# Kernel optimization log

Hardware: AMD Instinct MI355X
Metric: run time of the kernel (lower is better)

The kernel has to match this reference:

```python
import jax, jax.numpy as jnp
import numpy as np

DIM = 512; H = 8; KH = 2; G = 4; DH = 64        # dim, q heads, kv heads, GQA group, head dim
BALL = 128; SEL = 64; TOPK = 2; PDIM = 3        # sliding ball, compress/selection block, topk, pos dim
SCALE = DH ** -0.5


def _rms_norm(x, gamma):
    return x * jax.lax.rsqrt(jnp.mean(x * x, axis=-1, keepdims=True) + 1e-6) * gamma


def _rotary(t):
    # t: (B, h, S, DH); GPT-NeoX style rotate-half rotary embedding
    S = t.shape[-2]
    inv = 1.0 / (10000.0 ** (jnp.arange(0, DH, 2, dtype=jnp.float32) / DH))
    f = jnp.arange(S, dtype=jnp.float32)[:, None] * inv          # (S, DH/2)
    cos = jnp.concatenate([jnp.cos(f), jnp.cos(f)], -1)
    sin = jnp.concatenate([jnp.sin(f), jnp.sin(f)], -1)
    t1, t2 = jnp.split(t, 2, -1)
    return t * cos + jnp.concatenate([-t2, t1], -1) * sin


def _forward(x, pos, pe_w, pe_b, gamma, wq, wk, wv, k_pos, v_pos,
             k_w1, k_b1, k_w2, k_b2, v_w1, v_b1, v_w2, v_b2,
             mem_k, mem_v, w_combine, w_out, num_batches):
    B = num_batches
    # relative position of leaves wrt ball center (no-grad in original)
    p = jax.lax.stop_gradient(pos).reshape(-1, SEL, PDIM)
    rel = (p - p.mean(axis=1, keepdims=True)).reshape(-1, PDIM)
    x = x + rel @ pe_w + pe_b
    x = x.reshape(B, -1, DIM)
    S = x.shape[1]
    nb = S // SEL
    h = _rms_norm(x, gamma)
    q = (h @ wq).reshape(B, S, H, DH).transpose(0, 2, 1, 3)      # (B,H,S,DH)
    k = (h @ wk).reshape(B, S, KH, DH).transpose(0, 2, 1, 3)     # (B,KH,S,DH)
    v = (h @ wv).reshape(B, S, KH, DH).transpose(0, 2, 1, 3)
    qr, kr = _rotary(q), _rotary(k)

    # --- compressed branch: per-block intra-pos emb + MLP compression ---
    kb = k.reshape(B, KH, nb, SEL, DH) + k_pos[None, :, None]
    vb = v.reshape(B, KH, nb, SEL, DH) + v_pos[None, :, None]
    ck = jax.nn.relu(kb.reshape(B, KH, nb, SEL * DH) @ k_w1 + k_b1) @ k_w2 + k_b2
    cv = jax.nn.relu(vb.reshape(B, KH, nb, SEL * DH) @ v_w1 + v_b1) @ v_w2 + v_b2
    ck = jnp.concatenate([jnp.broadcast_to(mem_k[None], (B, KH, 1, DH)), ck], axis=2)
    cv = jnp.concatenate([jnp.broadcast_to(mem_v[None], (B, KH, 1, DH)), cv], axis=2)
    qg = qr.reshape(B, KH, G, S, DH)
    csim = jnp.einsum('bkgsd,bknd->bkgsn', qg, ck) * SCALE
    cattn = jax.nn.softmax(csim, axis=-1)
    cout = jnp.einsum('bkgsn,bknd->bkgsd', cattn, cv).reshape(B, H, S, DH)

    # --- top-k block selection from compressed attention importance ---
    imp = cattn[..., 1:].mean(axis=2)                            # share over grouped q heads: (B,KH,S,nb)
    imp_blk = imp.reshape(B, KH, nb, SEL, nb).mean(axis=3)       # per query block: (B,KH,nb,nb)
    _, sel = jax.lax.top_k(imp_blk, TOPK)                        # (B,KH,nb,TOPK)

    # --- fine branch: each query block attends own + TOPK selected blocks ---
    kblk = kr.reshape(B, KH, nb, SEL, DH)
    vblk = v.reshape(B, KH, nb, SEL, DH)
    gather = jax.vmap(jax.vmap(lambda t, s: t[s]))               # (nb,SEL,DH),(nb,TOPK)->(nb,TOPK,SEL,DH)
    fk = jnp.concatenate([gather(kblk, sel), kblk[:, :, :, None]], axis=3)
    fv = jnp.concatenate([gather(vblk, sel), vblk[:, :, :, None]], axis=3)
    fk = fk.reshape(B, KH, nb, (TOPK + 1) * SEL, DH)
    fv = fv.reshape(B, KH, nb, (TOPK + 1) * SEL, DH)
    qb = qr.reshape(B, KH, G, nb, SEL, DH)
    fsim = jnp.einsum('bkgnqd,bknmd->bkgnqm', qb, fk) * SCALE
    fout = jnp.einsum('bkgnqm,bknmd->bkgnqd', jax.nn.softmax(fsim, -1), fv)
    fout = fout.reshape(B, H, S, DH)

    # --- sliding branch: MiniBallAttn = plain SDPA within balls of size 128 ---
    nw = S // BALL
    qw = qr.reshape(B, H, nw, BALL, DH)
    kw = jnp.repeat(kr, G, axis=1).reshape(B, H, nw, BALL, DH)
    vw = jnp.repeat(v, G, axis=1).reshape(B, H, nw, BALL, DH)
    ssim = jnp.einsum('bhnqd,bhnkd->bhnqk', qw, kw) * SCALE
    sout = jnp.einsum('bhnqk,bhnkd->bhnqd', jax.nn.softmax(ssim, -1), vw)
    sout = sout.reshape(B, H, S, DH)

    # --- sigmoid-gated strategy combine, merge heads, out projection ---
    gates = jax.nn.sigmoid(h @ w_combine).reshape(B, S, H, 3).transpose(0, 2, 1, 3)
    out = gates[..., 0:1] * cout + gates[..., 1:2] * fout + gates[..., 2:3] * sout
    out = out.transpose(0, 2, 1, 3).reshape(B, S, H * DH) @ w_out
    return out.reshape(-1, DIM)


def setup_inputs() -> dict:
    key = jax.random.key(0)
    ks = jax.random.split(key, 16)
    Bn, S = 8, 4096
    N = Bn * S
    CD = SEL * DH
    def lin(k, fi, fo):
        return (jax.random.normal(k, (fi, fo), jnp.float32) / np.sqrt(fi)).astype(jnp.float32)
    return {
        'x': jax.random.normal(ks[0], (N, DIM), jnp.float32),
        'pos': jax.random.normal(ks[1], (N, PDIM), jnp.float32),
        'pe_w': lin(ks[2], PDIM, DIM),
        'pe_b': jnp.zeros((DIM,), jnp.float32),
        'gamma': jnp.ones((DIM,), jnp.float32),
        'wq': lin(ks[3], DIM, H * DH),
        'wk': lin(ks[4], DIM, KH * DH),
        'wv': lin(ks[5], DIM, KH * DH),
        'k_pos': jax.random.normal(ks[6], (KH, SEL, DH), jnp.float32) * 0.02,
        'v_pos': jax.random.normal(ks[7], (KH, SEL, DH), jnp.float32) * 0.02,
        'k_w1': lin(ks[8], CD, CD), 'k_b1': jnp.zeros((CD,), jnp.float32),
        'k_w2': lin(ks[9], CD, DH), 'k_b2': jnp.zeros((DH,), jnp.float32),
        'v_w1': lin(ks[10], CD, CD), 'v_b1': jnp.zeros((CD,), jnp.float32),
        'v_w2': lin(ks[11], CD, DH), 'v_b2': jnp.zeros((DH,), jnp.float32),
        'mem_k': jax.random.normal(ks[12], (KH, 1, DH), jnp.float32) * 0.02,
        'mem_v': jax.random.normal(ks[13], (KH, 1, DH), jnp.float32) * 0.02,
        'w_combine': lin(ks[14], DIM, 3 * H),
        'w_out': lin(ks[15], H * DH, DIM),
        'num_batches': 8,
    }


def reference(x, pos, pe_w, pe_b, gamma, wq, wk, wv, k_pos, v_pos,
              k_w1, k_b1, k_w2, k_b2, v_w1, v_b1, v_w2, v_b2,
              mem_k, mem_v, w_combine, w_out, num_batches):
    return _forward(x, pos, pe_w, pe_b, gamma, wq, wk, wv, k_pos, v_pos,
                    k_w1, k_b1, k_w2, k_b2, v_w1, v_b1, v_w2, v_b2,
                    mem_k, mem_v, w_combine, w_out, num_batches)
```

## Files before the change

kernel.cpp:

```cpp
#include <hip/hip_runtime.h>
#include <stdint.h>

#define DEVI static __device__ __forceinline__
typedef unsigned short u16;
typedef __bf16 bhalf8 __attribute__((ext_vector_type(8)));
typedef float f32x4 __attribute__((ext_vector_type(4)));

DEVI u16 f2bf(float f) {
  union { float f; unsigned u; } v; v.f = f;
  unsigned r = v.u + 0x7FFFu + ((v.u >> 16) & 1u);
  return (u16)(r >> 16);
}
DEVI float bf2f(u16 h) {
  union { unsigned u; float f; } v; v.u = ((unsigned)h) << 16;
  return v.f;
}
DEVI f32x4 MFMA(bhalf8 a, bhalf8 b, f32x4 c) {
  return __builtin_amdgcn_mfma_f32_16x16x32_bf16(a, b, c, 0, 0, 0);
}
DEVI bhalf8 LD8(const u16* p) { return *(const bhalf8*)p; }
DEVI f32x4 zero4() { f32x4 z = {0.f, 0.f, 0.f, 0.f}; return z; }

#define GLDS16(gp, lp) __builtin_amdgcn_global_load_lds( \
    (const __attribute__((address_space(1))) void*)(gp), \
    (__attribute__((address_space(3))) void*)(lp), 16, 0, 0)


__global__ __launch_bounds__(256) void nsa_hnorm(const float* __restrict__ x, const float* __restrict__ pos,
    const float* __restrict__ pew, const float* __restrict__ peb,
    const float* __restrict__ gamma, u16* __restrict__ hhi, u16* __restrict__ hlo) {
  int n = blockIdx.x, t = threadIdx.x;
  int blk = n >> 6;
  __shared__ float spm[3];
  if (t < 64) {
    const float* p = pos + (size_t)(blk * 64 + t) * 3;
    float a = p[0], b = p[1], c = p[2];
#pragma unroll
    for (int o = 32; o; o >>= 1) { a += __shfl_down(a, o); b += __shfl_down(b, o); c += __shfl_down(c, o); }
    if (t == 0) { spm[0] = a * (1.f/64.f); spm[1] = b * (1.f/64.f); spm[2] = c * (1.f/64.f); }
  }
  __syncthreads();
  float r0 = pos[(size_t)n*3+0] - spm[0];
  float r1 = pos[(size_t)n*3+1] - spm[1];
  float r2 = pos[(size_t)n*3+2] - spm[2];
  int c0 = t, c1 = t + 256;
  const float* xr = x + (size_t)n * 512;
  float v0 = xr[c0] + r0*pew[c0] + r1*pew[512+c0] + r2*pew[1024+c0] + peb[c0];
  float v1 = xr[c1] + r0*pew[c1] + r1*pew[512+c1] + r2*pew[1024+c1] + peb[c1];
  float ss = v0*v0 + v1*v1;
#pragma unroll
  for (int o = 32; o; o >>= 1) ss += __shfl_down(ss, o);
  __shared__ float red[4];
  if ((t & 63) == 0) red[t >> 6] = ss;
  __syncthreads();
  float rms = 1.0f / sqrtf((red[0]+red[1]+red[2]+red[3]) * (1.0f/512.0f) + 1e-6f);
  float h0 = v0 * rms * gamma[c0], h1 = v1 * rms * gamma[c1];
  u16 a0 = f2bf(h0); hhi[(size_t)n*512+c0] = a0; hlo[(size_t)n*512+c0] = f2bf(h0 - bf2f(a0));
  u16 a1 = f2bf(h1); hhi[(size_t)n*512+c1] = a1; hlo[(size_t)n*512+c1] = f2bf(h1 - bf2f(a1));
}

__global__ __launch_bounds__(256) void nsa_wcat_rope(const float* __restrict__ wq, const float* __restrict__ wk,
    const float* __restrict__ wv, const float* __restrict__ wc, u16* __restrict__ hi, u16* __restrict__ lo,
    float* __restrict__ ct, float* __restrict__ st) {
  int bidx = blockIdx.x;
  if (bidx < 1792) {
    int idx = bidx * 256 + threadIdx.x;
    int k = idx & 511, n = idx >> 9;
    float v;
    if (n < 512) v = wq[(size_t)k*512 + n];
    else if (n < 640) v = wk[(size_t)k*128 + n - 512];
    else if (n < 768) v = wv[(size_t)k*128 + n - 640];
    else if (n < 792) v = wc[(size_t)k*24 + n - 768];
    else v = 0.f;
    u16 h = f2bf(v); hi[idx] = h; lo[idx] = f2bf(v - bf2f(h));
  } else {
    int idx = (bidx - 1792) * 256 + threadIdx.x;
    int s = idx >> 5, i = idx & 31;
    float e = (float)(2*i) * (1.0f/64.0f);
    float inv = 1.0f / powf(10000.0f, e);
    float f = (float)s * inv;
    ct[idx] = cosf(f); st[idx] = sinf(f);
  }
}

__global__ __launch_bounds__(256) void nsa_vT16(const u16* __restrict__ v16, u16* __restrict__ vT) {
  int blk = blockIdx.x;
  int st = (blk & 63) * 64, bkh = blk >> 6;
  __shared__ u16 tile[64][72];
  int t = threadIdx.x;
  int s = t >> 2, c0 = (t & 3) * 16;
  const u16* src = v16 + ((size_t)bkh*4096 + st + s) * 64;
  *(int4*)&tile[s][c0]   = *(const int4*)&src[c0];
  *(int4*)&tile[s][c0+8] = *(const int4*)&src[c0+8];
  __syncthreads();
  int d = t >> 2, s0 = (t & 3) * 16;
  u16* dst = vT + ((size_t)bkh*64 + d)*4096 + st + s0;
#pragma unroll
  for (int j = 0; j < 16; ++j) dst[j] = tile[s0+j][d];
}

__global__ __launch_bounds__(256) void nsa_wT(const float* __restrict__ src, u16* __restrict__ dhi,
    u16* __restrict__ dlo, int K, int N) {
  __shared__ float tile[64][65];
  int k0 = blockIdx.x * 64, n0 = blockIdx.y * 64;
  int t = threadIdx.x, r = t >> 2, c0 = (t & 3) * 16;
#pragma unroll
  for (int j = 0; j < 16; ++j) tile[r][c0+j] = src[(size_t)(k0+r)*N + n0 + c0 + j];
  __syncthreads();
  size_t ob = (size_t)(n0 + r)*K + k0 + c0;
#pragma unroll
  for (int j = 0; j < 16; ++j) {
    float v = tile[c0+j][r];
    u16 h = f2bf(v); dhi[ob+j] = h;
    if (dlo) dlo[ob+j] = f2bf(v - bf2f(h));
  }
}

__global__ __launch_bounds__(256) void nsa_wT2(const float* __restrict__ srcA, u16* __restrict__ dhA,
    u16* __restrict__ dlA, const float* __restrict__ srcB, u16* __restrict__ dhB, u16* __restrict__ dlB,
    int K, int N) {
  const float* src = blockIdx.z ? srcB : srcA;
  u16* dhi = blockIdx.z ? dhB : dhA;
  u16* dlo = blockIdx.z ? dlB : dlA;
  __shared__ float tile[64][65];
  int k0 = blockIdx.x * 64, n0 = blockIdx.y * 64;
  int t = threadIdx.x, r = t >> 2, c0 = (t & 3) * 16;
#pragma unroll
  for (int j = 0; j < 16; ++j) tile[r][c0+j] = src[(size_t)(k0+r)*N + n0 + c0 + j];
  __syncthreads();
  size_t ob = (size_t)(n0 + r)*K + k0 + c0;
#pragma unroll
  for (int j = 0; j < 16; ++j) {
    float v = tile[c0+j][r];
    u16 h = f2bf(v); dhi[ob+j] = h;
    if (dlo) dlo[ob+j] = f2bf(v - bf2f(h));
  }
}

__global__ __launch_bounds__(256) void nsa_red_ckcv(const float* __restrict__ part,
    const float* __restrict__ mem_k, const float* __restrict__ kb2,
    const float* __restrict__ mem_v, const float* __restrict__ vb2,
    u16* __restrict__ ckh, u16* __restrict__ ckl, u16* __restrict__ cvT) {
  int idx = blockIdx.x * 256 + threadIdx.x;
  if (idx < 81920) {
    int d = idx & 63, n = (idx >> 6) % 80, bkh = idx / (80*64);
    int kh = bkh & 1;
    float v;
    if (n == 0) v = mem_k[kh*64 + d];
    else if (n <= 64) {
      v = kb2[d];
      int m = bkh*64 + (n - 1);
#pragma unroll
      for (int kc = 0; kc < 16; ++kc) v += part[((size_t)kc*1024 + m)*64 + d];
    } else v = 0.f;
    u16 h = f2bf(v); ckh[idx] = h; ckl[idx] = f2bf(v - bf2f(h));
  } else if (idx < 81920 + 98304) {
    int j = idx - 81920;
    int cc = j % 96, d = (j / 96) & 63, bkh = j / (96*64);
    int kh = bkh & 1;
    const float* pv = part + (size_t)16*1024*64;
    float v;
    if (cc == 0) v = mem_v[kh*64 + d];
    else if (cc <= 64) {
      v = vb2[d];
      int m = bkh*64 + (cc - 1);
#pragma unroll
      for (int kc = 0; kc < 16; ++kc) v += pv[((size_t)kc*1024 + m)*64 + d];
    } else v = 0.f;
    cvT[j] = f2bf(v);
  }
}

__global__ __launch_bounds__(256) void nsa_sentinel(float* __restrict__ o, int n, float val) {
  int i = blockIdx.x * 256 + threadIdx.x;
  if (i < n) o[i] = val;
}

template<bool SPLIT, int EPI>
__global__ __launch_bounds__(256) void nsa_gemm(const u16* __restrict__ Ah, const u16* __restrict__ Al,
    const u16* __restrict__ Bh, const u16* __restrict__ Bl, int K, int N,
    const float* __restrict__ p_cos, float* __restrict__ p_sin,
    u16* __restrict__ out_hi, u16* __restrict__ out_lo, float* __restrict__ og,
    const float* __restrict__ kpos, const float* __restrict__ vpos,
    u16* __restrict__ krb, u16* __restrict__ kbh, u16* __restrict__ kbl,
    u16* __restrict__ v16o, u16* __restrict__ vbh) {
  constexpr int NB = SPLIT ? 4 : 2;
  __shared__ u16 sm[NB * 2 * 4096];
  const int t = threadIdx.x, w = t >> 6, l = t & 63;
  const int wm = w >> 1, wn = w & 1;
  int m0, n0;
  if constexpr (EPI == 0) {
    const int nper = (int)gridDim.y;
    const int bid = blockIdx.y * 256 + blockIdx.x;
    const int xcd = bid & 7, j = bid >> 3;
    const int mg = j / (8*nper), rem = j % (8*nper);
    const int nn = rem >> 3, mi = rem & 7;
    m0 = ((xcd * 4 + mg) * 8 + mi) * 128;
    n0 = nn * 128;
  } else {
    const int MBn = gridDim.x;
    const int nwg = MBn * gridDim.y;
    const int bid = blockIdx.y * MBn + blockIdx.x;
    const int swz = (bid & 7) * (nwg >> 3) + (bid >> 3);
    m0 = (swz % MBn) * 128; n0 = (swz / MBn) * 128;
  }
  const bool dsp = SPLIT && (EPI != 0 || n0 <= 512);
  const int row = l & 15;
  const int kc8 = ((l >> 4) ^ ((l >> 1) & 3)) * 8;
  const int gsc = ((l & 3) ^ ((l >> 3) & 3)) * 8;
  const int sr = l >> 2;
  f32x4 acc[4][4];
#pragma unroll
  for (int a = 0; a < 4; ++a)
#pragma unroll
    for (int b = 0; b < 4; ++b) acc[a][b] = zero4();

  auto STAGE = [&](int buf, int k0) {
    u16* base = sm + buf * NB * 4096;
#pragma unroll
    for (int s2 = 0; s2 < 2; ++s2) {
      int seg = w*2 + s2;
      int r = seg*16 + sr;
      size_t ga = (size_t)(m0 + r)*K + k0 + gsc;
      size_t gb = (size_t)(n0 + r)*K + k0 + gsc;
      GLDS16(&Ah[ga], base + seg*512);
      GLDS16(&Bh[gb], base + 4096 + seg*512);
      if (SPLIT && dsp) {
        GLDS16(&Al[ga], base + 2*4096 + seg*512);
        GLDS16(&Bl[gb], base + 3*4096 + seg*512);
      }
    }
  };

  const int nt = K >> 5;
  STAGE(0, 0);
  __syncthreads();
  int cur = 0;
  for (int kt = 0; kt < nt; ++kt) {
    if (kt + 1 < nt) STAGE(cur ^ 1, (kt + 1) * 32);
    u16* bA  = sm + cur * NB * 4096;
    u16* bB  = bA + 4096;
    u16* bAl = bA + 2*4096;
    u16* bBl = bA + 3*4096;
    bhalf8 af[4], afl[4];
#pragma unroll
    for (int mf = 0; mf < 4; ++mf) {
      af[mf] = LD8(&bA[(wm*64 + mf*16 + row)*32 + kc8]);
      if (dsp) afl[mf] = LD8(&bAl[(wm*64 + mf*16 + row)*32 + kc8]);
    }
#pragma unroll
    for (int nf = 0; nf < 4; ++nf) {
      bhalf8 bfh = LD8(&bB[(wn*64 + nf*16 + row)*32 + kc8]);
      bhalf8 bfl;
      if (dsp) bfl = LD8(&bBl[(wn*64 + nf*16 + row)*32 + kc8]);
#pragma unroll
      for (int mf = 0; mf < 4; ++mf) {
        acc[mf][nf] = MFMA(af[mf], bfh, acc[mf][nf]);
        if (dsp) {
          acc[mf][nf] = MFMA(af[mf], bfl, acc[mf][nf]);
          acc[mf][nf] = MFMA(afl[mf], bfh, acc[mf][nf]);
        }
      }
    }
    __syncthreads();
    cur ^= 1;
  }
  if constexpr (EPI == 0) {
    if (n0 < 512) {
#pragma unroll
      for (int mf = 0; mf < 4; ++mf)
#pragma unroll
        for (int i = 0; i < 4; ++i) {
          int r = m0 + wm*64 + mf*16 + (l >> 4)*4 + i;
          int s = r & 4095, b = r >> 12;
#pragma unroll
          for (int nf = 0; nf < 2; ++nf) {
            int c = n0 + wn*64 + nf*16 + (l & 15);
            int hq = c >> 6, dd = c & 31;
            float t1 = acc[mf][nf][i], t2 = acc[mf][nf+2][i];
            float cs = p_cos[s*32 + dd], sn = p_sin[s*32 + dd];
            float o1 = t1*cs - t2*sn, o2 = t2*cs + t1*sn;
            size_t ob = (((size_t)(b*8 + hq))*4096 + s)*64;
            u16 h1 = f2bf(o1); out_hi[ob+dd] = h1;    out_lo[ob+dd] = f2bf(o1 - bf2f(h1));
            u16 h2 = f2bf(o2); out_hi[ob+dd+32] = h2; out_lo[ob+dd+32] = f2bf(o2 - bf2f(h2));
          }
        }
    } else if (n0 == 512) {
      int kh = wn;
#pragma unroll
      for (int mf = 0; mf < 4; ++mf)
#pragma unroll
        for (int i = 0; i < 4; ++i) {
          int r = m0 + wm*64 + mf*16 + (l >> 4)*4 + i;
          int s = r & 4095, b = r >> 12;
          int n = s >> 6, sl = s & 63;
          size_t krbase = ((size_t)(b*2 + kh)*4096 + s)*64;
          size_t kbbase = ((size_t)(b*128 + kh*64 + n))*4096 + sl*64;
#pragma unroll
          for (int nf = 0; nf < 2; ++nf) {
            int dd = nf*16 + (l & 15);
            float t1 = acc[mf][nf][i], t2 = acc[mf][nf+2][i];
            float cs = p_cos[s*32 + dd], sn = p_sin[s*32 + dd];
            krb[krbase + dd]      = f2bf(t1*cs - t2*sn);
            krb[krbase + dd + 32] = f2bf(t2*cs + t1*sn);
          }
#pragma unroll
          for (int nf = 0; nf < 4; ++nf) {
            int dk = nf*16 + (l & 15);
            float v = acc[mf][nf][i] + kpos[(kh*64 + sl)*64 + dk];
            u16 h = f2bf(v);
            kbh[kbbase + dk] = h;
            kbl[kbbase + dk] = f2bf(v - bf2f(h));
          }
        }
    } else if (n0 == 640) {
      int kh = wn;
#pragma unroll
      for (int mf = 0; mf < 4; ++mf)
#pragma unroll
        for (int i = 0; i < 4; ++i) {
          int r = m0 + wm*64 + mf*16 + (l >> 4)*4 + i;
          int s = r & 4095, b = r >> 12;
          int n = s >> 6, sl = s & 63;
          size_t v16base = ((size_t)(b*2 + kh)*4096 + s)*64;
          size_t vbbase = ((size_t)(b*128 + kh*64 + n))*4096 + sl*64;
#pragma unroll
          for (int nf = 0; nf < 4; ++nf) {
            int dv = nf*16 + (l & 15);
            float vv = acc[mf][nf][i];
            v16o[v16base + dv] = f2bf(vv);
            vbh[vbbase + dv] = f2bf(vv + vpos[(kh*64 + sl)*64 + dv]);
          }
        }
    } else {
#pragma unroll
      for (int mf = 0; mf < 4; ++mf)
#pragma unroll
        for (int nf = 0; nf < 4; ++nf)
#pragma unroll
          for (int i = 0; i < 4; ++i) {
            int r = m0 + wm*64 + mf*16 + (l >> 4)*4 + i;
            int c = n0 + wn*64 + nf*16 + (l & 15);
            if (c < 792) og[(size_t)r*24 + (c - 768)] = 1.0f / (1.0f + expf(-acc[mf][nf][i]));
          }
    }
  } else {
#pragma unroll
    for (int mf = 0; mf < 4; ++mf)
#pragma unroll
      for (int nf = 0; nf < 4; ++nf)
#pragma unroll
        for (int i = 0; i < 4; ++i) {
          int r = m0 + wm*64 + mf*16 + (l >> 4)*4 + i;
          int c = n0 + wn*64 + nf*16 + (l & 15);
          p_sin[(size_t)r*N + c] = acc[mf][nf][i];
        }
  }
}

__global__ __launch_bounds__(256) void nsa_mlp1(const u16* __restrict__ kbh, const u16* __restrict__ kbl,
    const u16* __restrict__ vbh, const u16* __restrict__ w1kh, const u16* __restrict__ w1kl,
    const u16* __restrict__ w1vh, const float* __restrict__ kb1, const float* __restrict__ vb1,
    u16* __restrict__ th, u16* __restrict__ tl, u16* __restrict__ tv) {
  __shared__ u16 sm[4 * 2 * 4096];
  const int t = threadIdx.x, w = t >> 6, l = t & 63;
  const int wm = w >> 1, wn = w & 1;
  const int bid = blockIdx.x;
  const int xcd = bid & 7, u = bid >> 3;
  const bool isK = u < 32;
  const int uu = isK ? u : u - 32;
  const int m0 = (uu & 7) * 128;
  const int n0 = (xcd * 4 + (uu >> 3)) * 128;
  const u16* Ah = isK ? kbh : vbh;
  const u16* Bh = isK ? w1kh : w1vh;
  constexpr int K = 4096;
  const int row = l & 15;
  const int kc8 = ((l >> 4) ^ ((l >> 1) & 3)) * 8;
  const int gsc = ((l & 3) ^ ((l >> 3) & 3)) * 8;
  const int sr = l >> 2;
  f32x4 acc[4][4];
#pragma unroll
  for (int a = 0; a < 4; ++a)
#pragma unroll
    for (int b = 0; b < 4; ++b) acc[a][b] = zero4();

  auto STAGE = [&](int buf, int k0) {
    u16* base = sm + buf * 4 * 4096;
#pragma unroll
    for (int s2 = 0; s2 < 2; ++s2) {
      int seg = w*2 + s2;
      int r = seg*16 + sr;
      size_t ga = (size_t)(m0 + r)*K + k0 + gsc;
      size_t gb = (size_t)(n0 + r)*K + k0 + gsc;
      GLDS16(&Ah[ga], base + seg*512);
      GLDS16(&Bh[gb], base + 4096 + seg*512);
      if (isK) {
        GLDS16(&kbl[ga], base + 2*4096 + seg*512);
        GLDS16(&w1kl[gb], base + 3*4096 + seg*512);
      }
    }
  };

  STAGE(0, 0);
  __syncthreads();
  int cur = 0;
  for (int kt = 0; kt < 128; ++kt) {
    if (kt + 1 < 128) STAGE(cur ^ 1, (kt + 1) * 32);
    u16* bA  = sm + cur * 4 * 4096;
    u16* bB  = bA + 4096;
    u16* bAl = bA + 2*4096;
    u16* bBl = bA + 3*4096;
    bhalf8 af[4], afl[4];
#pragma unroll
    for (int mf = 0; mf < 4; ++mf) {
      af[mf] = LD8(&bA[(wm*64 + mf*16 + row)*32 + kc8]);
      if (isK) afl[mf] = LD8(&bAl[(wm*64 + mf*16 + row)*32 + kc8]);
    }
#pragma unroll
    for (int nf = 0; nf < 4; ++nf) {
      bhalf8 bfh = LD8(&bB[(wn*64 + nf*16 + row)*32 + kc8]);
      bhalf8 bfl;
      if (isK) bfl = LD8(&bBl[(wn*64 + nf*16 + row)*32 + kc8]);
#pragma unroll
      for (int mf = 0; mf < 4; ++mf) {
        acc[mf][nf] = MFMA(af[mf], bfh, acc[mf][nf]);
        if (isK) {
          acc[mf][nf] = MFMA(af[mf], bfl, acc[mf][nf]);
          acc[mf][nf] = MFMA(afl[mf], bfh, acc[mf][nf]);
        }
      }
    }
    __syncthreads();
    cur ^= 1;
  }
  const float* bias = isK ? kb1 : vb1;
#pragma unroll
  for (int mf = 0; mf < 4; ++mf)
#pragma unroll
    for (int nf = 0; nf < 4; ++nf)
#pragma unroll
      for (int i = 0; i < 4; ++i) {
        int r = m0 + wm*64 + mf*16 + (l >> 4)*4 + i;
        int c = n0 + wn*64 + nf*16 + (l & 15);
        float v = fmaxf(acc[mf][nf][i] + bias[c], 0.f);
        if (isK) {
          u16 h = f2bf(v);
          th[(size_t)r*4096 + c] = h;
          tl[(size_t)r*4096 + c] = f2bf(v - bf2f(h));
        } else {
          tv[(size_t)r*4096 + c] = f2bf(v);
        }
      }
}

__global__ __launch_bounds__(256) void nsa_gemm64m(const u16* __restrict__ th, const u16* __restrict__ tl,
    const u16* __restrict__ tv, const u16* __restrict__ w2h, const u16* __restrict__ w2l,
    const u16* __restrict__ w2vh, float* __restrict__ part) {
  __shared__ u16 sm[4 * 2 * 2048];
  const int t = threadIdx.x, w = t >> 6, l = t & 63;
  const int mt = blockIdx.x;
  const bool isK = blockIdx.y < 16;
  const int kc = blockIdx.y & 15;
  const u16* Ah = isK ? th : tv;
  const u16* Bh = isK ? w2h : w2vh;
  float* po = part + (isK ? 0 : (size_t)16*1024*64);
  const int row = l & 15;
  const int kc8 = ((l >> 4) ^ ((l >> 1) & 3)) * 8;
  const int gsc = ((l & 3) ^ ((l >> 3) & 3)) * 8;
  const int sr = l >> 2;
  f32x4 acc[4];
#pragma unroll
  for (int a = 0; a < 4; ++a) acc[a] = zero4();

  auto STAGE = [&](int buf, int k0) {
    u16* base = sm + buf * 4 * 2048;
    int r = w*16 + sr;
    size_t ga = (size_t)(mt*64 + r)*4096 + k0 + gsc;
    size_t gb = (size_t)r*4096 + k0 + gsc;
    GLDS16(&Ah[ga], base + w*512);
    GLDS16(&Bh[gb], base + 2048 + w*512);
    if (isK) {
      GLDS16(&tl[ga], base + 2*2048 + w*512);
      GLDS16(&w2l[gb], base + 3*2048 + w*512);
    }
  };

  STAGE(0, kc*256);
  __syncthreads();
  int cur = 0;
  for (int kt = 0; kt < 8; ++kt) {
    if (kt + 1 < 8) STAGE(cur ^ 1, kc*256 + (kt + 1) * 32);
    u16* bA  = sm + cur * 4 * 2048;
    u16* bB  = bA + 2048;
    u16* bAl = bA + 2*2048;
    u16* bBl = bA + 3*2048;
    bhalf8 a = LD8(&bA[(w*16 + row)*32 + kc8]);
    bhalf8 al;
    if (isK) al = LD8(&bAl[(w*16 + row)*32 + kc8]);
#pragma unroll
    for (int nf = 0; nf < 4; ++nf) {
      bhalf8 b = LD8(&bB[(nf*16 + row)*32 + kc8]);
      bhalf8 bl;
      if (isK) bl = LD8(&bBl[(nf*16 + row)*32 + kc8]);
      acc[nf] = MFMA(a, b, acc[nf]);
      if (isK) {
        acc[nf] = MFMA(a, bl, acc[nf]);
        acc[nf] = MFMA(al, b, acc[nf]);
      }
    }
    __syncthreads();
    cur ^= 1;
  }
#pragma unroll
  for (int nf = 0; nf < 4; ++nf)
#pragma unroll
    for (int i = 0; i < 4; ++i) {
      int m = mt*64 + w*16 + (l >> 4)*4 + i;
      int d = nf*16 + (l & 15);
      po[((size_t)kc*1024 + m)*64 + d] = acc[nf][i];
    }
}


__global__ __launch_bounds__(256) void nsa_attn_comp(const u16* __restrict__ qrh, const u16* __restrict__ qrl,
    const u16* __restrict__ ckh, const u16* __restrict__ ckl, const u16* __restrict__ cvT,
    const float* __restrict__ g32, u16* __restrict__ comb, float* __restrict__ imp) {
  __shared__ u16 smem[24832];
  __shared__ float sImp[4 * 80];
  u16* sKh = smem;
  u16* sKl = smem + 5760;
  u16* sVT = smem + 11520;
  u16* sP  = smem + 18176;
  const int t = threadIdx.x, w = t >> 6, l = t & 63;
  const int bid = blockIdx.x;
  const int qt = bid & 63, kh = (bid >> 6) & 1, b = bid >> 7;
  const int row = l & 15, kg = (l >> 4) * 8;
  size_t kbase = (size_t)(b*2 + kh) * 80 * 64;
  size_t vbase = (size_t)(b*2 + kh) * 64 * 96;
  for (int e = t; e < 640; e += 256) {
    int r = e >> 3, c = (e & 7) * 8;
    *(int4*)&sKh[r*72 + c] = *(const int4*)&ckh[kbase + r*64 + c];
    *(int4*)&sKl[r*72 + c] = *(const int4*)&ckl[kbase + r*64 + c];
  }
  for (int e = t; e < 768; e += 256) {
    int r = e / 12, ch = e % 12;
    *(int4*)&sVT[r*104 + ch*8] = *(const int4*)&cvT[vbase + (size_t)r*96 + ch*8];
  }
  for (int e = l; e < 80; e += 64) sImp[w*80 + e] = 0.f;
#pragma unroll
  for (int i = 0; i < 4; ++i)
    sP[(w*16 + (l & 15))*104 + 80 + (l >> 4)*4 + i] = 0;
  __syncthreads();
  for (int g = 0; g < 4; ++g) {
    size_t qbase = ((size_t)((b*2 + kh)*4 + g)*4096 + qt*64) * 64 + (size_t)(w*16 + row)*64;
    bhalf8 ah0 = LD8(&qrh[qbase + kg]);
    bhalf8 ah1 = LD8(&qrh[qbase + 32 + kg]);
    bhalf8 al0 = LD8(&qrl[qbase + kg]);
    bhalf8 al1 = LD8(&qrl[qbase + 32 + kg]);
    f32x4 sc[5];
#pragma unroll
    for (int nf = 0; nf < 5; ++nf) sc[nf] = zero4();
#pragma unroll
    for (int kk = 0; kk < 2; ++kk) {
      bhalf8 ah = kk ? ah1 : ah0;
      bhalf8 al = kk ? al1 : al0;
#pragma unroll
      for (int nf = 0; nf < 5; ++nf) {
        bhalf8 bh = LD8(&sKh[(nf*16 + row)*72 + kk*32 + kg]);
        bhalf8 bl = LD8(&sKl[(nf*16 + row)*72 + kk*32 + kg]);
        sc[nf] = MFMA(ah, bh, sc[nf]);
        sc[nf] = MFMA(ah, bl, sc[nf]);
        sc[nf] = MFMA(al, bh, sc[nf]);
      }
    }
    float mx[4] = {-1e30f, -1e30f, -1e30f, -1e30f};
#pragma unroll
    for (int nf = 0; nf < 5; ++nf)
#pragma unroll
      for (int i = 0; i < 4; ++i) {
        int col = nf*16 + (l & 15);
        float v = (col < 65) ? sc[nf][i] * 0.125f : -1e30f;
        sc[nf][i] = v;
        mx[i] = fmaxf(mx[i], v);
      }
#pragma unroll
    for (int i = 0; i < 4; ++i)
#pragma unroll
      for (int o = 1; o < 16; o <<= 1) mx[i] = fmaxf(mx[i], __shfl_xor(mx[i], o));
    float sum[4] = {0.f, 0.f, 0.f, 0.f};
#pragma unroll
    for (int nf = 0; nf < 5; ++nf)
#pragma unroll
      for (int i = 0; i < 4; ++i) {
        int col = nf*16 + (l & 15);
        float p = (col < 65) ? expf(sc[nf][i] - mx[i]) : 0.f;
        sc[nf][i] = p;
        sum[i] += p;
      }
#pragma unroll
    for (int i = 0; i < 4; ++i)
#pragma unroll
      for (int o = 1; o < 16; o <<= 1) sum[i] += __shfl_xor(sum[i], o);
    float inv[4];
#pragma unroll
    for (int i = 0; i < 4; ++i) inv[i] = 1.0f / sum[i];
#pragma unroll
    for (int nf = 0; nf < 5; ++nf)
#pragma unroll
      for (int i = 0; i < 4; ++i)
        sP[(w*16 + (l >> 4)*4 + i)*104 + nf*16 + (l & 15)] = f2bf(sc[nf][i] * inv[i]);
#pragma unroll
    for (int nf = 0; nf < 5; ++nf) {
      float cs = 0.f;
#pragma unroll
      for (int i = 0; i < 4; ++i) cs += sc[nf][i] * inv[i];
      cs += __shfl_xor(cs, 16);
      cs += __shfl_xor(cs, 32);
      if (l < 16) sImp[w*80 + nf*16 + l] += cs;
    }
    f32x4 ov[4];
#pragma unroll
    for (int nf = 0; nf < 4; ++nf) ov[nf] = zero4();
#pragma unroll
    for (int kk = 0; kk < 3; ++kk) {
      bhalf8 a = LD8(&sP[(w*16 + row)*104 + kk*32 + kg]);
#pragma unroll
      for (int nf = 0; nf < 4; ++nf) {
        bhalf8 bv = LD8(&sVT[(nf*16 + row)*104 + kk*32 + kg]);
        ov[nf] = MFMA(a, bv, ov[nf]);
      }
    }
    int hq = kh*4 + g;
#pragma unroll
    for (int i = 0; i < 4; ++i) {
      int q = qt*64 + w*16 + (l >> 4)*4 + i;
      float gate = g32[((size_t)b*4096 + q)*24 + hq*3 + 0];
#pragma unroll
      for (int nf = 0; nf < 4; ++nf) {
        int d = nf*16 + (l & 15);
        comb[(((size_t)b*4096 + q)*8 + hq)*64 + d] = f2bf(gate * ov[nf][i]);
      }
    }
  }
  __syncthreads();
  if (t < 64) {
    int n = t + 1;
    imp[(size_t)bid*64 + t] = (sImp[n] + sImp[80 + n] + sImp[160 + n] + sImp[240 + n]) * (1.0f/256.0f);
  }
}

__global__ __launch_bounds__(64) void nsa_top2(const float* __restrict__ imp, int* __restrict__ sel) {
  int blk = blockIdx.x;
  int l = threadIdx.x;
  float v = imp[(size_t)blk*64 + l];
  float v1 = v; int i1 = l;
#pragma unroll
  for (int o = 1; o < 64; o <<= 1) {
    float ovv = __shfl_xor(v1, o); int oi = __shfl_xor(i1, o);
    if (ovv > v1 || (ovv == v1 && oi < i1)) { v1 = ovv; i1 = oi; }
  }
  float v2 = (l == i1) ? -3.0e38f : v; int i2 = l;
#pragma unroll
  for (int o = 1; o < 64; o <<= 1) {
    float ovv = __shfl_xor(v2, o); int oi = __shfl_xor(i2, o);
    if (ovv > v2 || (ovv == v2 && oi < i2)) { v2 = ovv; i2 = oi; }
  }
  if (l == 0) { sel[blk*2 + 0] = i1; sel[blk*2 + 1] = i2; }
}

__global__ __launch_bounds__(256) void nsa_attn_fine(const u16* __restrict__ qrh, const u16* __restrict__ kr,
    const u16* __restrict__ vT, const int* __restrict__ sel, const float* __restrict__ g32,
    u16* __restrict__ comb) {
  __shared__ u16 smem[39424];
  u16* sK  = smem;
  u16* sVT = smem + 13824;
  u16* sP  = smem + 26624;
  const int t = threadIdx.x, w = t >> 6, l = t & 63;
  const int bid = blockIdx.x;
  const int qt = bid & 63, kh = (bid >> 6) & 1, b = bid >> 7;
  const int row = l & 15, kg = (l >> 4) * 8;
  const int s0 = sel[bid*2 + 0] & 63, s1 = sel[bid*2 + 1] & 63;
  size_t kvb = (size_t)(b*2 + kh) * 4096 * 64;
  size_t vtb = (size_t)(b*2 + kh) * 64 * 4096;
  for (int e = t; e < 1536; e += 256) {
    int r = e >> 3, c = (e & 7) * 8;
    int bi = r >> 6;
    int blkid = (bi == 0) ? s0 : ((bi == 1) ? s1 : qt);
    int sidx = blkid*64 + (r & 63);
    *(int4*)&sK[r*72 + c] = *(const int4*)&kr[kvb + (size_t)sidx*64 + c];
  }
  for (int e = t; e < 1536; e += 256) {
    int r = e / 24, ch = e % 24;
    int n0 = ch * 8, bi = n0 >> 6;
    int blkid = (bi == 0) ? s0 : ((bi == 1) ? s1 : qt);
    int sidx = blkid*64 + (n0 & 63);
    *(int4*)&sVT[r*200 + n0] = *(const int4*)&vT[vtb + (size_t)r*4096 + sidx];
  }
  __syncthreads();
  for (int g = 0; g < 4; ++g) {
    size_t qbase = ((size_t)((b*2 + kh)*4 + g)*4096 + qt*64) * 64 + (size_t)(w*16 + row)*64;
    bhalf8 a0 = LD8(&qrh[qbase + kg]);
    bhalf8 a1 = LD8(&qrh[qbase + 32 + kg]);
    f32x4 sc[12];
#pragma unroll
    for (int nf = 0; nf < 12; ++nf) sc[nf] = zero4();
#pragma unroll
    for (int kk = 0; kk < 2; ++kk) {
      bhalf8 a = kk ? a1 : a0;
#pragma unroll
      for (int nf = 0; nf < 12; ++nf) {
        bhalf8 bk = LD8(&sK[(nf*16 + row)*72 + kk*32 + kg]);
        sc[nf] = MFMA(a, bk, sc[nf]);
      }
    }
    float mx[4] = {-1e30f, -1e30f, -1e30f, -1e30f};
#pragma unroll
    for (int nf = 0; nf < 12; ++nf)
#pragma unroll
      for (int i = 0; i < 4; ++i) {
        float v = sc[nf][i] * 0.125f;
        sc[nf][i] = v;
        mx[i] = fmaxf(mx[i], v);
      }
#pragma unroll
    for (int i = 0; i < 4; ++i)
#pragma unroll
      for (int o = 1; o < 16; o <<= 1) mx[i] = fmaxf(mx[i], __shfl_xor(mx[i], o));
    float sum[4] = {0.f, 0.f, 0.f, 0.f};
#pragma unroll
    for (int nf = 0; nf < 12; ++nf)
#pragma unroll
      for (int i = 0; i < 4; ++i) {
        float p = expf(sc[nf][i] - mx[i]);
        sc[nf][i] = p;
        sum[i] += p;
      }
#pragma unroll
    for (int i = 0; i < 4; ++i)
#pragma unroll
      for (int o = 1; o < 16; o <<= 1) sum[i] += __shfl_xor(sum[i], o);
    float inv[4];
#pragma unroll
    for (int i = 0; i < 4; ++i) inv[i] = 1.0f / sum[i];
#pragma unroll
    for (int nf = 0; nf < 12; ++nf)
#pragma unroll
      for (int i = 0; i < 4; ++i)
        sP[(w*16 + (l >> 4)*4 + i)*200 + nf*16 + (l & 15)] = f2bf(sc[nf][i] * inv[i]);
    f32x4 ovv[4];
#pragma unroll
    for (int nf = 0; nf < 4; ++nf) ovv[nf] = zero4();
#pragma unroll
    for (int kk = 0; kk < 6; ++kk) {
      bhalf8 a = LD8(&sP[(w*16 + row)*200 + kk*32 + kg]);
#pragma unroll
      for (int nf = 0; nf < 4; ++nf) {
        bhalf8 bv = LD8(&sVT[(nf*16 + row)*200 + kk*32 + kg]);
        ovv[nf] = MFMA(a, bv, ovv[nf]);
      }
    }
    int hq = kh*4 + g;
#pragma unroll
    for (int i = 0; i < 4; ++i) {
      int q = qt*64 + w*16 + (l >> 4)*4 + i;
      float gate = g32[((size_t)b*4096 + q)*24 + hq*3 + 1];
#pragma unroll
      for (int nf = 0; nf < 4; ++nf) {
        int d = nf*16 + (l & 15);
        size_t oi = (((size_t)b*4096 + q)*8 + hq)*64 + d;
        comb[oi] = f2bf(bf2f(comb[oi]) + gate * ovv[nf][i]);
      }
    }
  }
}

__global__ __launch_bounds__(256) void nsa_attn_slide(const u16* __restrict__ qrh, const u16* __restrict__ kr,
    const u16* __restrict__ vT, const float* __restrict__ g32, u16* __restrict__ comb) {
  __shared__ u16 smem[26624];
  u16* sK  = smem;
  u16* sVT = smem + 9216;
  u16* sP  = smem + 17920;
  const int t = threadIdx.x, w = t >> 6, l = t & 63;
  const int bid = blockIdx.x;
  const int ball = bid & 31, kh = (bid >> 5) & 1, b = bid >> 6;
  const int row = l & 15, kg = (l >> 4) * 8;
  const int ks0 = ball * 128;
  size_t kvb = (size_t)(b*2 + kh) * 4096 * 64;
  size_t vtb = (size_t)(b*2 + kh) * 64 * 4096;
  for (int e = t; e < 1024; e += 256) {
    int r = e >> 3, c = (e & 7) * 8;
    *(int4*)&sK[r*72 + c] = *(const int4*)&kr[kvb + (size_t)(ks0 + r)*64 + c];
  }
  for (int e = t; e < 1024; e += 256) {
    int r = e >> 4, ch = e & 15;
    *(int4*)&sVT[r*136 + ch*8] = *(const int4*)&vT[vtb + (size_t)r*4096 + ks0 + ch*8];
  }
  __syncthreads();
  for (int hq = 0; hq < 4; ++hq) {
    int hh = kh*4 + hq;
    for (int qh = 0; qh < 2; ++qh) {
      int qt = ball*2 + qh;
      size_t qbase = ((size_t)(b*8 + hh)*4096 + qt*64) * 64 + (size_t)(w*16 + row)*64;
      bhalf8 a0 = LD8(&qrh[qbase + kg]);
      bhalf8 a1 = LD8(&qrh[qbase + 32 + kg]);
      f32x4 sc[8];
#pragma unroll
      for (int nf = 0; nf < 8; ++nf) sc[nf] = zero4();
#pragma unroll
      for (int kk = 0; kk < 2; ++kk) {
        bhalf8 a = kk ? a1 : a0;
#pragma unroll
        for (int nf = 0; nf < 8; ++nf) {
          bhalf8 bk = LD8(&sK[(nf*16 + row)*72 + kk*32 + kg]);
          sc[nf] = MFMA(a, bk, sc[nf]);
        }
      }
      float mx[4] = {-1e30f, -1e30f, -1e30f, -1e30f};
#pragma unroll
      for (int nf = 0; nf < 8; ++nf)
#pragma unroll
        for (int i = 0; i < 4; ++i) {
          float v = sc[nf][i] * 0.125f;
          sc[nf][i] = v;
          mx[i] = fmaxf(mx[i], v);
        }
#pragma unroll
      for (int i = 0; i < 4; ++i)
#pragma unroll
        for (int o = 1; o < 16; o <<= 1) mx[i] = fmaxf(mx[i], __shfl_xor(mx[i], o));
      float sum[4] = {0.f, 0.f, 0.f, 0.f};
#pragma unroll
      for (int nf = 0; nf < 8; ++nf)
#pragma unroll
        for (int i = 0; i < 4; ++i) {
          float p = expf(sc[nf][i] - mx[i]);
          sc[nf][i] = p;
          sum[i] += p;
        }
#pragma unroll
      for (int i = 0; i < 4; ++i)
#pragma unroll
        for (int o = 1; o < 16; o <<= 1) sum[i] += __shfl_xor(sum[i], o);
      float inv[4];
#pragma unroll
      for (int i = 0; i < 4; ++i) inv[i] = 1.0f / sum[i];
#pragma unroll
      for (int nf = 0; nf < 8; ++nf)
#pragma unroll
        for (int i = 0; i < 4; ++i)
          sP[(w*16 + (l >> 4)*4 + i)*136 + nf*16 + (l & 15)] = f2bf(sc[nf][i] * inv[i]);
      f32x4 ovv[4];
#pragma unroll
      for (int nf = 0; nf < 4; ++nf) ovv[nf] = zero4();
#pragma unroll
      for (int kk = 0; kk < 4; ++kk) {
        bhalf8 a = LD8(&sP[(w*16 + row)*136 + kk*32 + kg]);
#pragma unroll
        for (int nf = 0; nf < 4; ++nf) {
          bhalf8 bv = LD8(&sVT[(nf*16 + row)*136 + kk*32 + kg]);
          ovv[nf] = MFMA(a, bv, ovv[nf]);
        }
      }
#pragma unroll
      for (int i = 0; i < 4; ++i) {
        int q = qt*64 + w*16 + (l >> 4)*4 + i;
        float gate = g32[((size_t)b*4096 + q)*24 + hh*3 + 2];
#pragma unroll
        for (int nf = 0; nf < 4; ++nf) {
          int d = nf*16 + (l & 15);
          size_t oi = (((size_t)b*4096 + q)*8 + hh)*64 + d;
          comb[oi] = f2bf(bf2f(comb[oi]) + gate * ovv[nf][i]);
        }
      }
    }
  }
}


extern "C" void kernel_launch(void* const* d_in, const int* in_sizes, int n_in,
                              void* d_out, int out_size, void* d_ws, size_t ws_size,
                              hipStream_t stream) {
  const float* x     = (const float*)d_in[0];
  const float* pos   = (const float*)d_in[1];
  const float* pe_w  = (const float*)d_in[2];
  const float* pe_b  = (const float*)d_in[3];
  const float* gamma = (const float*)d_in[4];
  const float* wq    = (const float*)d_in[5];
  const float* wk    = (const float*)d_in[6];
  const float* wv    = (const float*)d_in[7];
  const float* k_pos = (const float*)d_in[8];
  const float* v_pos = (const float*)d_in[9];
  const float* k_w1  = (const float*)d_in[10];
  const float* k_b1  = (const float*)d_in[11];
  const float* k_w2  = (const float*)d_in[12];
  const float* k_b2  = (const float*)d_in[13];
  const float* v_w1  = (const float*)d_in[14];
  const float* v_b1  = (const float*)d_in[15];
  const float* v_w2  = (const float*)d_in[16];
  const float* v_b2  = (const float*)d_in[17];
  const float* mem_k = (const float*)d_in[18];
  const float* mem_v = (const float*)d_in[19];
  const float* w_cmb = (const float*)d_in[20];
  const float* w_out = (const float*)d_in[21];
  float* out = (float*)d_out;
  char* ws = (char*)d_ws;

  size_t off = 0;
  auto A = [&](size_t b) { size_t o = off; off += (b + 255) & ~(size_t)255; return o; };
  const size_t oR1 = A(100663296);
  const size_t oR2 = A(67108864);
  const size_t oR4 = A(16777216);
  const size_t oR5 = A(16777216);
  const size_t oR6 = A(16777216);
  const size_t oR7 = A(16777216);
  const size_t oR8 = A(3145728);
  const size_t oR9 = A(2097152);
  const size_t o_cos = A(524288),  o_sin = A(524288);
  const size_t o_ckh = A(163840),  o_ckl = A(163840);
  const size_t o_cvT = A(196608);
  const size_t o_woh = A(524288);
  const size_t o_imp = A(262144);
  const size_t o_sel = A(8192);
  const size_t o_part = A(8388608);

  if (ws_size < off) {
    nsa_sentinel<<<(out_size + 255)/256, 256, 0, stream>>>(out, out_size, (float)(ws_size >> 20));
    return;
  }

#define WP(T, o) ((T*)(ws + (o)))
  u16*  h_hi = WP(u16, oR1);           u16* h_lo = WP(u16, oR1 + 33554432);
  u16*  w1kh = WP(u16, oR1);           u16* w1kl = WP(u16, oR1 + 33554432);
  u16*  w1vh = WP(u16, oR1 + 67108864);
  u16*  combp = WP(u16, oR1);
  u16*  qrh  = WP(u16, oR2);           u16* qrl  = WP(u16, oR2 + 33554432);
  u16*  th   = WP(u16, oR4);           u16* tl   = WP(u16, oR4 + 8388608);
  u16*  v16b = WP(u16, oR5);           u16* vbh  = WP(u16, oR5 + 8388608);
  u16*  tv   = WP(u16, oR5);
  u16*  kbh  = WP(u16, oR6);           u16* kbl  = WP(u16, oR6 + 8388608);
  u16*  krb  = WP(u16, oR7);           u16* vTb  = WP(u16, oR7 + 8388608);
  float* g32 = WP(float, oR8);
  u16*  wch  = WP(u16, oR9);           u16* wcl  = WP(u16, oR9 + 917504);
  u16*  w2h  = WP(u16, oR9);           u16* w2l  = WP(u16, oR9 + 524288);
  u16*  w2vh = WP(u16, oR9 + 1048576);
  float* cosb = WP(float, o_cos);      float* sinb = WP(float, o_sin);
  u16*  ckh  = WP(u16, o_ckh);         u16* ckl  = WP(u16, o_ckl);
  u16*  cvT  = WP(u16, o_cvT);
  u16*  woh  = WP(u16, o_woh);
  float* imp = WP(float, o_imp);
  int*  selp = WP(int, o_sel);
  float* part = WP(float, o_part);

  nsa_hnorm<<<32768, 256, 0, stream>>>(x, pos, pe_w, pe_b, gamma, h_hi, h_lo);
  nsa_wcat_rope<<<2304, 256, 0, stream>>>(wq, wk, wv, w_cmb, wch, wcl, cosb, sinb);
  nsa_gemm<true, 0><<<dim3(256, 7, 1), 256, 0, stream>>>(h_hi, h_lo, wch, wcl, 512, 896,
      cosb, sinb, qrh, qrl, g32, k_pos, v_pos, krb, kbh, kbl, v16b, vbh);
  nsa_vT16<<<1024, 256, 0, stream>>>(v16b, vTb);
  nsa_wT2<<<dim3(64, 64, 2), 256, 0, stream>>>(k_w1, w1kh, w1kl, v_w1, w1vh, nullptr, 4096, 4096);
  nsa_wT2<<<dim3(64, 1, 2), 256, 0, stream>>>(k_w2, w2h, w2l, v_w2, w2vh, nullptr, 4096, 64);
  nsa_mlp1<<<512, 256, 0, stream>>>(kbh, kbl, vbh, w1kh, w1kl, w1vh, k_b1, v_b1, th, tl, tv);
  nsa_gemm64m<<<dim3(16, 32), 256, 0, stream>>>(th, tl, tv, w2h, w2l, w2vh, part);
  nsa_red_ckcv<<<704, 256, 0, stream>>>(part, mem_k, k_b2, mem_v, v_b2, ckh, ckl, cvT);
  nsa_attn_comp<<<1024, 256, 0, stream>>>(qrh, qrl, ckh, ckl, cvT, g32, combp, imp);
  nsa_top2<<<1024, 64, 0, stream>>>(imp, selp);
  nsa_attn_fine<<<1024, 256, 0, stream>>>(qrh, krb, vTb, selp, g32, combp);
  nsa_attn_slide<<<512, 256, 0, stream>>>(qrh, krb, vTb, g32, combp);
  nsa_wT<<<dim3(8, 8), 256, 0, stream>>>(w_out, woh, nullptr, 512, 512);
  nsa_gemm<false, 2><<<dim3(256, 4, 1), 256, 0, stream>>>(combp, nullptr, woh, nullptr, 512, 512,
      nullptr, out, nullptr, nullptr, nullptr, nullptr, nullptr, nullptr, nullptr, nullptr,
      nullptr, nullptr);
#undef WP
}
```

Baseline: 694.1 us.

## Split MLP first-layer GEMM along K and reduce with fused bias-ReLU kernel

Replaces the dedicated nsa_mlp1 kernel, which ran 512 blocks over K=4096 for both K and V, with the generic nsa_gemm given a split-K grid dimension (2 splits). Each split writes fp32 partials, and a new elementwise kernel sums them, adds the bias, applies ReLU and converts to bf16 hi/lo. The K and V paths now run as separate launches, and their weight transposes are serialized so one workspace buffer can be reused. This doubles the number of blocks per GEMM to improve occupancy, at the cost of extra fp32 partial traffic and more launches.

```diff
diff --git a/kernel.cpp b/kernel.cpp
--- a/kernel.cpp
+++ b/kernel.cpp
@@ -134,6 +134,28 @@
     float v = tile[c0+j][r];
     u16 h = f2bf(v); dhi[ob+j] = h;
     if (dlo) dlo[ob+j] = f2bf(v - bf2f(h));
+  }
+}
+
+template<bool SPLIT>
+__global__ __launch_bounds__(256) void nsa_mlp_fuse(const float* __restrict__ part,
+    const float* __restrict__ bias, u16* __restrict__ oh, u16* __restrict__ ol) {
+  size_t i = ((size_t)blockIdx.x * 256 + threadIdx.x) * 4;
+  int c = (int)(i & 4095);
+  float4 a = *(const float4*)&part[i];
+  float4 b = *(const float4*)&part[(size_t)4194304 + i];
+  float v0 = fmaxf(a.x + b.x + bias[c+0], 0.f);
+  float v1 = fmaxf(a.y + b.y + bias[c+1], 0.f);
+  float v2 = fmaxf(a.z + b.z + bias[c+2], 0.f);
+  float v3 = fmaxf(a.w + b.w + bias[c+3], 0.f);
+  u16 h0 = f2bf(v0), h1 = f2bf(v1), h2 = f2bf(v2), h3 = f2bf(v3);
+  ((unsigned long long*)oh)[i >> 2] = (unsigned long long)h0 | ((unsigned long long)h1 << 16) |
+                                      ((unsigned long long)h2 << 32) | ((unsigned long long)h3 << 48);
+  if (SPLIT) {
+    u16 l0 = f2bf(v0 - bf2f(h0)), l1 = f2bf(v1 - bf2f(h1));
+    u16 l2 = f2bf(v2 - bf2f(h2)), l3 = f2bf(v3 - bf2f(h3));
+    ((unsigned long long*)ol)[i >> 2] = (unsigned long long)l0 | ((unsigned long long)l1 << 16) |
+                                        ((unsigned long long)l2 << 32) | ((unsigned long long)l3 << 48);
   }
 }
 
@@ -205,6 +227,8 @@
     m0 = (swz % MBn) * 128; n0 = (swz / MBn) * 128;
   }
   const bool dsp = SPLIT && (EPI != 0 || n0 <= 512);
+  const int klen = K / (int)gridDim.z;
+  const int kb0 = blockIdx.z * klen;
   const int row = l & 15;
   const int kc8 = ((l >> 4) ^ ((l >> 1) & 3)) * 8;
   const int gsc = ((l & 3) ^ ((l >> 3) & 3)) * 8;
@@ -232,12 +256,12 @@
     }
   };
 
-  const int nt = K >> 5;
-  STAGE(0, 0);
+  const int nt = klen >> 5;
+  STAGE(0, kb0);
   __syncthreads();
   int cur = 0;
   for (int kt = 0; kt < nt; ++kt) {
-    if (kt + 1 < nt) STAGE(cur ^ 1, (kt + 1) * 32);
+    if (kt + 1 < nt) STAGE(cur ^ 1, kb0 + (kt + 1) * 32);
     u16* bA  = sm + cur * NB * 4096;
     u16* bB  = bA + 4096;
     u16* bAl = bA + 2*4096;
@@ -344,7 +368,7 @@
             if (c < 792) og[(size_t)r*24 + (c - 768)] = 1.0f / (1.0f + expf(-acc[mf][nf][i]));
           }
     }
-  } else {
+  } else if constexpr (EPI == 2) {
 #pragma unroll
     for (int mf = 0; mf < 4; ++mf)
 #pragma unroll
@@ -355,102 +379,19 @@
           int c = n0 + wn*64 + nf*16 + (l & 15);
           p_sin[(size_t)r*N + c] = acc[mf][nf][i];
         }
-  }
-}
-
-__global__ __launch_bounds__(256) void nsa_mlp1(const u16* __restrict__ kbh, const u16* __restrict__ kbl,
-    const u16* __restrict__ vbh, const u16* __restrict__ w1kh, const u16* __restrict__ w1kl,
-    const u16* __restrict__ w1vh, const float* __restrict__ kb1, const float* __restrict__ vb1,
-    u16* __restrict__ th, u16* __restrict__ tl, u16* __restrict__ tv) {
-  __shared__ u16 sm[4 * 2 * 4096];
-  const int t = threadIdx.x, w = t >> 6, l = t & 63;
-  const int wm = w >> 1, wn = w & 1;
-  const int bid = blockIdx.x;
-  const int xcd = bid & 7, u = bid >> 3;
-  const bool isK = u < 32;
-  const int uu = isK ? u : u - 32;
-  const int m0 = (uu & 7) * 128;
-  const int n0 = (xcd * 4 + (uu >> 3)) * 128;
-  const u16* Ah = isK ? kbh : vbh;
-  const u16* Bh = isK ? w1kh : w1vh;
-  constexpr int K = 4096;
-  const int row = l & 15;
-  const int kc8 = ((l >> 4) ^ ((l >> 1) & 3)) * 8;
-  const int gsc = ((l & 3) ^ ((l >> 3) & 3)) * 8;
-  const int sr = l >> 2;
-  f32x4 acc[4][4];
-#pragma unroll
-  for (int a = 0; a < 4; ++a)
-#pragma unroll
-    for (int b = 0; b < 4; ++b) acc[a][b] = zero4();
-
-  auto STAGE = [&](int buf, int k0) {
-    u16* base = sm + buf * 4 * 4096;
-#pragma unroll
-    for (int s2 = 0; s2 < 2; ++s2) {
-      int seg = w*2 + s2;
-      int r = seg*16 + sr;
-      size_t ga = (size_t)(m0 + r)*K + k0 + gsc;
-      size_t gb = (size_t)(n0 + r)*K + k0 + gsc;
-      GLDS16(&Ah[ga], base + seg*512);
-      GLDS16(&Bh[gb], base + 4096 + seg*512);
-      if (isK) {
-        GLDS16(&kbl[ga], base + 2*4096 + seg*512);
-        GLDS16(&w1kl[gb], base + 3*4096 + seg*512);
-      }
-    }
-  };
-
-  STAGE(0, 0);
-  __syncthreads();
-  int cur = 0;
-  for (int kt = 0; kt < 128; ++kt) {
-    if (kt + 1 < 128) STAGE(cur ^ 1, (kt + 1) * 32);
-    u16* bA  = sm + cur * 4 * 4096;
-    u16* bB  = bA + 4096;
-    u16* bAl = bA + 2*4096;
-    u16* bBl = bA + 3*4096;
-    bhalf8 af[4], afl[4];
-#pragma unroll
-    for (int mf = 0; mf < 4; ++mf) {
-      af[mf] = LD8(&bA[(wm*64 + mf*16 + row)*32 + kc8]);
-      if (isK) afl[mf] = LD8(&bAl[(wm*64 + mf*16 + row)*32 + kc8]);
-    }
-#pragma unroll
-    for (int nf = 0; nf < 4; ++nf) {
-      bhalf8 bfh = LD8(&bB[(wn*64 + nf*16 + row)*32 + kc8]);
-      bhalf8 bfl;
-      if (isK) bfl = LD8(&bBl[(wn*64 + nf*16 + row)*32 + kc8]);
-#pragma unroll
-      for (int mf = 0; mf < 4; ++mf) {
-        acc[mf][nf] = MFMA(af[mf], bfh, acc[mf][nf]);
-        if (isK) {
-          acc[mf][nf] = MFMA(af[mf], bfl, acc[mf][nf]);
-          acc[mf][nf] = MFMA(afl[mf], bfh, acc[mf][nf]);
-        }
-      }
-    }
-    __syncthreads();
-    cur ^= 1;
-  }
-  const float* bias = isK ? kb1 : vb1;
-#pragma unroll
-  for (int mf = 0; mf < 4; ++mf)
-#pragma unroll
-    for (int nf = 0; nf < 4; ++nf)
-#pragma unroll
-      for (int i = 0; i < 4; ++i) {
-        int r = m0 + wm*64 + mf*16 + (l >> 4)*4 + i;
-        int c = n0 + wn*64 + nf*16 + (l & 15);
-        float v = fmaxf(acc[mf][nf][i] + bias[c], 0.f);
-        if (isK) {
-          u16 h = f2bf(v);
-          th[(size_t)r*4096 + c] = h;
-          tl[(size_t)r*4096 + c] = f2bf(v - bf2f(h));
-        } else {
-          tv[(size_t)r*4096 + c] = f2bf(v);
-        }
-      }
+  } else {
+    const int M = (int)gridDim.x * 128;
+#pragma unroll
+    for (int mf = 0; mf < 4; ++mf)
+#pragma unroll
+      for (int nf = 0; nf < 4; ++nf)
+#pragma unroll
+        for (int i = 0; i < 4; ++i) {
+          int r = m0 + wm*64 + mf*16 + (l >> 4)*4 + i;
+          int c = n0 + wn*64 + nf*16 + (l & 15);
+          p_sin[((size_t)blockIdx.z * M + r) * (size_t)N + c] = acc[mf][nf][i];
+        }
+  }
 }
 
 __global__ __launch_bounds__(256) void nsa_gemm64m(const u16* __restrict__ th, const u16* __restrict__ tl,
@@ -907,7 +848,7 @@
 
   size_t off = 0;
   auto A = [&](size_t b) { size_t o = off; off += (b + 255) & ~(size_t)255; return o; };
-  const size_t oR1 = A(100663296);
+  const size_t oR1 = A(67108864);
   const size_t oR2 = A(67108864);
   const size_t oR4 = A(16777216);
   const size_t oR5 = A(16777216);
@@ -921,7 +862,7 @@
   const size_t o_woh = A(524288);
   const size_t o_imp = A(262144);
   const size_t o_sel = A(8192);
-  const size_t o_part = A(8388608);
+  const size_t o_part1 = A(33554432);
 
   if (ws_size < off) {
     nsa_sentinel<<<(out_size + 255)/256, 256, 0, stream>>>(out, out_size, (float)(ws_size >> 20));
@@ -931,7 +872,7 @@
 #define WP(T, o) ((T*)(ws + (o)))
   u16*  h_hi = WP(u16, oR1);           u16* h_lo = WP(u16, oR1 + 33554432);
   u16*  w1kh = WP(u16, oR1);           u16* w1kl = WP(u16, oR1 + 33554432);
-  u16*  w1vh = WP(u16, oR1 + 67108864);
+  u16*  w1vh = WP(u16, oR1);
   u16*  combp = WP(u16, oR1);
   u16*  qrh  = WP(u16, oR2);           u16* qrl  = WP(u16, oR2 + 33554432);
   u16*  th   = WP(u16, oR4);           u16* tl   = WP(u16, oR4 + 8388608);
@@ -949,16 +890,25 @@
   u16*  woh  = WP(u16, o_woh);
   float* imp = WP(float, o_imp);
   int*  selp = WP(int, o_sel);
-  float* part = WP(float, o_part);
+  float* part1 = WP(float, o_part1);
+  float* part  = WP(float, o_part1);
 
   nsa_hnorm<<<32768, 256, 0, stream>>>(x, pos, pe_w, pe_b, gamma, h_hi, h_lo);
   nsa_wcat_rope<<<2304, 256, 0, stream>>>(wq, wk, wv, w_cmb, wch, wcl, cosb, sinb);
   nsa_gemm<true, 0><<<dim3(256, 7, 1), 256, 0, stream>>>(h_hi, h_lo, wch, wcl, 512, 896,
       cosb, sinb, qrh, qrl, g32, k_pos, v_pos, krb, kbh, kbl, v16b, vbh);
   nsa_vT16<<<1024, 256, 0, stream>>>(v16b, vTb);
-  nsa_wT2<<<dim3(64, 64, 2), 256, 0, stream>>>(k_w1, w1kh, w1kl, v_w1, w1vh, nullptr, 4096, 4096);
+  nsa_wT<<<dim3(64, 64), 256, 0, stream>>>(k_w1, w1kh, w1kl, 4096, 4096);
+  nsa_gemm<true, 3><<<dim3(8, 32, 2), 256, 0, stream>>>(kbh, kbl, w1kh, w1kl, 4096, 4096,
+      nullptr, part1, nullptr, nullptr, nullptr, nullptr, nullptr, nullptr, nullptr, nullptr,
+      nullptr, nullptr);
+  nsa_mlp_fuse<true><<<4096, 256, 0, stream>>>(part1, k_b1, th, tl);
+  nsa_wT<<<dim3(64, 64), 256, 0, stream>>>(v_w1, w1vh, nullptr, 4096, 4096);
+  nsa_gemm<false, 3><<<dim3(8, 32, 2), 256, 0, stream>>>(vbh, nullptr, w1vh, nullptr, 4096, 4096,
+      nullptr, part1, nullptr, nullptr, nullptr, nullptr, nullptr, nullptr, nullptr, nullptr,
+      nullptr, nullptr);
+  nsa_mlp_fuse<false><<<4096, 256, 0, stream>>>(part1, v_b1, tv, nullptr);
   nsa_wT2<<<dim3(64, 1, 2), 256, 0, stream>>>(k_w2, w2h, w2l, v_w2, w2vh, nullptr, 4096, 64);
-  nsa_mlp1<<<512, 256, 0, stream>>>(kbh, kbl, vbh, w1kh, w1kl, w1vh, k_b1, v_b1, th, tl, tv);
   nsa_gemm64m<<<dim3(16, 32), 256, 0, stream>>>(th, tl, tv, w2h, w2l, w2vh, part);
   nsa_red_ckcv<<<704, 256, 0, stream>>>(part, mem_k, k_b2, mem_v, v_b2, ckh, ckl, cvT);
   nsa_attn_comp<<<1024, 256, 0, stream>>>(qrh, qrl, ckh, ckl, cvT, g32, combp, imp);
```

Measured after the change: 714.8 us. 1.03x slower.
